# Optimization experiments

Hardware: AMD Instinct MI355X
Metric: run time of the kernel (lower is better)

Reference implementation:

```python
import jax, jax.numpy as jnp
import numpy as np


def _dF(field, c):
    """Central differences of component c of field [B,X,Y,Z,C] -> [B,X-2,Y-2,Z-2,3]."""
    f = field[..., c]
    dx = (f[:, 2:, 1:-1, 1:-1] - f[:, :-2, 1:-1, 1:-1]) * 0.5
    dy = (f[:, 1:-1, 2:, 1:-1] - f[:, 1:-1, :-2, 1:-1]) * 0.5
    dz = (f[:, 1:-1, 1:-1, 2:] - f[:, 1:-1, 1:-1, :-2]) * 0.5
    return jnp.stack((dx, dy, dz), axis=4)


def setup_inputs() -> dict:
    key = jax.random.key(0)
    grid = jax.random.normal(key, (2, 160, 160, 160, 3), dtype=jnp.float32)
    return {"grid": grid}


def reference(grid):
    # First derivatives of each displacement component: [B,X-2,Y-2,Z-2,3]
    dx = _dF(grid, 0)
    dy = _dF(grid, 1)
    dz = _dF(grid, 2)
    # Second derivatives: [B,X-4,Y-4,Z-4,3]
    dxx = _dF(dx, 0)
    dyy = _dF(dy, 1)
    dzz = _dF(dz, 2)
    dxy = _dF(dx, 1)
    dyz = _dF(dy, 2)
    dxz = _dF(dx, 2)
    penalty = jnp.sum(dxx ** 2 + dyy ** 2 + dzz ** 2
                      + 2.0 * (dxy ** 2 + dyz ** 2 + dxz ** 2))
    return penalty / dxx.size
```

## Files before the change

### kernel.cpp

```cpp
#include <hip/hip_runtime.h>

#define OY 480
#define OX 76800
#define SB 12288000
#define JT 12
#define KQ 13
#define IT 12
#define NROW 16
#define ZST 60
#define RST 180
#define SLICE (NROW*RST)
#define CTHR (JT*KQ)
#define NGRP (NROW*14)
#define NBLK 1014
#define INV_SIZE (1.0f/22778496.0f)

__device__ __forceinline__ float4 ld4p(const float* p){ return *reinterpret_cast<const float4*>(p); }
__device__ __forceinline__ float2 ld2p(const float* p){ return *reinterpret_cast<const float2*>(p); }
__device__ __forceinline__ void st4p(float* p, float4 v){ *reinterpret_cast<float4*>(p) = v; }

#define STEP(P, V0a, V0b, DP) { \
    const int s = 2*d + (P); \
    const bool doLoad = stg && (s <= 14); \
    float4 A4, B4, C4; \
    if (doLoad) { \
        const float* gp = G + (size_t)(i0 - 1 + s)*OX + gbase; \
        A4 = ld4p(gp); B4 = ld4p(gp+4); C4 = ld4p(gp+8); \
    } \
    if (act) { \
        const bool doWS = (s >= 2) && (s <= 13); \
        const bool doXY = (s >= 3) && (s <= 14); \
        const bool doXX = (s >= 4); \
        const float* L = lds + (P)*SLICE; \
        float v0c[4], dz0[4], dz1[4], dz2[4], dyc0[4], dyc1[4]; \
        {  \
          float4 lo = ld4p(L+oj), hi = ld4p(L+oj+4); \
          float f[8] = {lo.x,lo.y,lo.z,lo.w,hi.x,hi.y,hi.z,hi.w}; \
          _Pragma("unroll") for (int v=0;v<4;++v){ v0c[v]=f[v+2]; dz0[v]=f[v+3]-f[v+1]; } \
          if (doWS) { \
            _Pragma("unroll") for (int v=0;v<4;++v){ float h=f[v+4]-2.f*f[v+2]+f[v]; cls2=fmaf(h,h,cls2); } \
            float2 pa=ld2p(L+oj+2*RST+2), pb=ld2p(L+oj+2*RST+4); \
            float2 ma=ld2p(L+oj-2*RST+2), mb=ld2p(L+oj-2*RST+4); \
            float hp[4]={pa.x,pa.y,pb.x,pb.y}, hm[4]={ma.x,ma.y,mb.x,mb.y}; \
            _Pragma("unroll") for (int v=0;v<4;++v){ float h=hp[v]-2.f*f[v+2]+hm[v]; cls2=fmaf(h,h,cls2); } \
          } \
        } \
        {  \
          float4 lo = ld4p(L+oj+ZST), hi = ld4p(L+oj+ZST+4); \
          float f[8] = {lo.x,lo.y,lo.z,lo.w,hi.x,hi.y,hi.z,hi.w}; \
          _Pragma("unroll") for (int v=0;v<4;++v){ dz1[v]=f[v+3]-f[v+1]; } \
          if (doWS) { \
            _Pragma("unroll") for (int v=0;v<4;++v){ float h=f[v+4]-2.f*f[v+2]+f[v]; cls2=fmaf(h,h,cls2); } \
            float2 pa=ld2p(L+oj+2*RST+ZST+2), pb=ld2p(L+oj+2*RST+ZST+4); \
            float2 ma=ld2p(L+oj-2*RST+ZST+2), mb=ld2p(L+oj-2*RST+ZST+4); \
            float hp[4]={pa.x,pa.y,pb.x,pb.y}, hm[4]={ma.x,ma.y,mb.x,mb.y}; \
            _Pragma("unroll") for (int v=0;v<4;++v){ float h=hp[v]-2.f*f[v+2]+hm[v]; cls1=fmaf(h,h,cls1); } \
          } \
        } \
        {  \
          float4 lo = ld4p(L+oj+2*ZST), hi = ld4p(L+oj+2*ZST+4); \
          float f[8] = {lo.x,lo.y,lo.z,lo.w,hi.x,hi.y,hi.z,hi.w}; \
          _Pragma("unroll") for (int v=0;v<4;++v){ dz2[v]=f[v+3]-f[v+1]; } \
          if (doWS) { \
            _Pragma("unroll") for (int v=0;v<4;++v){ float h=f[v+4]-2.f*f[v+2]+f[v]; cls1=fmaf(h,h,cls1); } \
          } \
        } \
        {  \
          float4 plo=ld4p(L+oj+RST), phi=ld4p(L+oj+RST+4); \
          float4 mlo=ld4p(L+oj-RST), mhi=ld4p(L+oj-RST+4); \
          float dyw[6]={plo.y-mlo.y, plo.z-mlo.z, plo.w-mlo.w, phi.x-mhi.x, phi.y-mhi.y, phi.z-mhi.z}; \
          _Pragma("unroll") for (int v=0;v<4;++v) dyc0[v]=dyw[v+1]; \
          if (doWS) { _Pragma("unroll") for (int v=0;v<4;++v){ float h=dyw[v+2]-dyw[v]; cls4=fmaf(h,h,cls4); } } \
        } \
        {  \
          float4 plo=ld4p(L+oj+RST+ZST), phi=ld4p(L+oj+RST+ZST+4); \
          float4 mlo=ld4p(L+oj-RST+ZST), mhi=ld4p(L+oj-RST+ZST+4); \
          float dyw[6]={plo.y-mlo.y, plo.z-mlo.z, plo.w-mlo.w, phi.x-mhi.x, phi.y-mhi.y, phi.z-mhi.z}; \
          _Pragma("unroll") for (int v=0;v<4;++v) dyc1[v]=dyw[v+1]; \
          if (doWS) { _Pragma("unroll") for (int v=0;v<4;++v){ float h=dyw[v+2]-dyw[v]; cls3=fmaf(h,h,cls3); } } \
        } \
        if (doWS) {  \
          float4 plo=ld4p(L+oj+RST+2*ZST), phi=ld4p(L+oj+RST+2*ZST+4); \
          float4 mlo=ld4p(L+oj-RST+2*ZST), mhi=ld4p(L+oj-RST+2*ZST+4); \
          float dyw[6]={plo.y-mlo.y, plo.z-mlo.z, plo.w-mlo.w, phi.x-mhi.x, phi.y-mhi.y, phi.z-mhi.z}; \
          _Pragma("unroll") for (int v=0;v<4;++v){ float h=dyw[v+2]-dyw[v]; cls1=fmaf(h,h,cls1); } \
        } \
        _Pragma("unroll") for (int v=0;v<4;++v) { \
          float o0=DP[0][v], o1=DP[1][v], o2=DP[2][v], o3=DP[3][v], o4=DP[4][v]; \
          if (doXY) { float h; \
            h=dyc0[v]-o0; cls3=fmaf(h,h,cls3); \
            h=dyc1[v]-o1; cls1=fmaf(h,h,cls1); \
            h=dz0[v]-o2;  cls3=fmaf(h,h,cls3); \
            h=dz1[v]-o3;  cls2=fmaf(h,h,cls2); \
            h=dz2[v]-o4;  cls1=fmaf(h,h,cls1); \
          } \
          DP[0][v]=dyc0[v]; DP[1][v]=dyc1[v]; DP[2][v]=dz0[v]; DP[3][v]=dz1[v]; DP[4][v]=dz2[v]; \
          float w2v=V0a[v], w4v=V0b[v]; \
          if (doXX) { float h=v0c[v]-2.f*w2v+w4v; cls1=fmaf(h,h,cls1); } \
          V0b[v]=w2v; V0a[v]=v0c[v]; \
        } \
    } \
    if (doLoad) { \
        float* Lw = lds + ((P)^1)*SLICE + lbase; \
        st4p(Lw,       make_float4(A4.x,A4.w,B4.z,C4.y)); \
        st4p(Lw+ZST,   make_float4(A4.y,B4.x,B4.w,C4.z)); \
        st4p(Lw+2*ZST, make_float4(A4.z,B4.y,C4.x,C4.w)); \
    } \
    __syncthreads(); \
}

__global__ __launch_bounds__(256)
void be_partials(const float* __restrict__ g, float* __restrict__ partial) {
    __shared__ float lds[2*SLICE];
    __shared__ float wsum[4];

    const int tid = threadIdx.x;
    const int bid = blockIdx.x;
    const int is = bid % 13;
    int r1 = bid / 13;
    const int kt = r1 % 3; r1 /= 3;
    const int jt = r1 % 13;
    const int bb = r1 / 13;

    const int j0  = 2 + jt*JT;
    const int zlo = 52*kt;
    const int i0  = 2 + is*IT;
    const float* __restrict__ G = g + (size_t)bb*SB;

    const bool stg = tid < NGRP;
    int gbase = 0, lbase = 0;
    if (stg) {
        int rr = tid/14, zq = tid - (tid/14)*14;
        gbase = (j0-2+rr)*OY + (zlo+4*zq)*3;
        lbase = rr*RST + 4*zq;
    }

    const bool act = tid < CTHR;
    int cj = tid/KQ, cq = tid - (tid/KQ)*KQ;
    if (!act) { cj = 0; cq = 0; }
    const int oj = (cj+2)*RST + 4*cq;

    float v0A0[4], v0A1[4], v0B0[4], v0B1[4];
    float dpA[5][4], dpB[5][4];
    #pragma unroll
    for (int v=0;v<4;++v){
        v0A0[v]=v0A1[v]=v0B0[v]=v0B1[v]=0.f;
        #pragma unroll
        for (int q=0;q<5;++q){ dpA[q][v]=0.f; dpB[q][v]=0.f; }
    }
    float cls1=0.f, cls2=0.f, cls3=0.f, cls4=0.f;

    if (stg) {
        const float* gp = G + (size_t)(i0-2)*OX + gbase;
        float4 A4 = ld4p(gp), B4 = ld4p(gp+4), C4 = ld4p(gp+8);
        float* Lw = lds + lbase;
        st4p(Lw,       make_float4(A4.x,A4.w,B4.z,C4.y));
        st4p(Lw+ZST,   make_float4(A4.y,B4.x,B4.w,C4.z));
        st4p(Lw+2*ZST, make_float4(A4.z,B4.y,C4.x,C4.w));
    }
    __syncthreads();

    #pragma unroll 1
    for (int d = 0; d < 8; ++d) {
        STEP(0, v0A0, v0A1, dpA)
        STEP(1, v0B0, v0B1, dpB)
    }

    float sv = fmaf(2.f, cls2, cls1);
    sv = fmaf(3.f, cls3, sv);
    sv = fmaf(4.f, cls4, sv);
    sv *= 0.0625f;

    #pragma unroll
    for (int off = 32; off > 0; off >>= 1) sv += __shfl_down(sv, off, 64);
    if ((tid & 63) == 0) wsum[tid >> 6] = sv;
    __syncthreads();
    if (tid == 0)
        partial[bid] = (wsum[0] + wsum[1]) + (wsum[2] + wsum[3]);
}

__global__ __launch_bounds__(256)
void be_final(const float* __restrict__ partial, float* __restrict__ out) {
    float s = 0.0f;
    for (int i = threadIdx.x; i < NBLK; i += 256) s += partial[i];
    #pragma unroll
    for (int off = 32; off > 0; off >>= 1) s += __shfl_down(s, off, 64);
    __shared__ float ws[4];
    if ((threadIdx.x & 63) == 0) ws[threadIdx.x >> 6] = s;
    __syncthreads();
    if (threadIdx.x == 0)
        out[0] = ((ws[0] + ws[1]) + (ws[2] + ws[3])) * INV_SIZE;
}

extern "C" void kernel_launch(void* const* d_in, const int* in_sizes, int n_in,
                              void* d_out, int out_size, void* d_ws, size_t ws_size,
                              hipStream_t stream) {
    const float* grid = (const float*)d_in[0];
    float* out = (float*)d_out;
    float* partials = (float*)d_ws;

    be_partials<<<dim3(NBLK), dim3(256), 0, stream>>>(grid, partials);
    be_final<<<1, 256, 0, stream>>>(partials, out);
}
```

Before: 177.7 us.

## Keep interleaved xyz layout in LDS and retile to full-Z row blocks

Stops de-interleaving the three displacement components into separate LDS planes and instead copies full contiguous Y-rows (all Z, interleaved components) straight into shared memory with flat float4 copies. Tiles now span the full Z extent with 6 Y-rows per block, giving 676 blocks of 234 compute threads instead of 1014 blocks of 156, with an occupancy hint of 3 blocks per CU. The aim is simpler, fully coalesced staging and better thread utilisation. In exchange each thread does wider LDS reads (24-float vectors), holds more registers, and staging now reads some redundant clamped data.

```diff
diff --git a/kernel.cpp b/kernel.cpp
--- a/kernel.cpp
+++ b/kernel.cpp
@@ -3,160 +3,156 @@
 #define OY 480
 #define OX 76800
 #define SB 12288000
-#define JT 12
-#define KQ 13
+#define JT 6
+#define NROW 10
 #define IT 12
-#define NROW 16
-#define ZST 60
-#define RST 180
-#define SLICE (NROW*RST)
-#define CTHR (JT*KQ)
-#define NGRP (NROW*14)
-#define NBLK 1014
+#define NSEG 13
+#define DATF4 1200
+#define SLICEF 5120
+#define CTHR 234
+#define NBLK 676
 #define INV_SIZE (1.0f/22778496.0f)
 
 __device__ __forceinline__ float4 ld4p(const float* p){ return *reinterpret_cast<const float4*>(p); }
-__device__ __forceinline__ float2 ld2p(const float* p){ return *reinterpret_cast<const float2*>(p); }
 __device__ __forceinline__ void st4p(float* p, float4 v){ *reinterpret_cast<float4*>(p) = v; }
+
+__device__ __forceinline__ void ld24(float* d, const float* p){
+    float4 x0=ld4p(p), x1=ld4p(p+4), x2=ld4p(p+8), x3=ld4p(p+12), x4=ld4p(p+16), x5=ld4p(p+20);
+    d[0]=x0.x; d[1]=x0.y; d[2]=x0.z; d[3]=x0.w;
+    d[4]=x1.x; d[5]=x1.y; d[6]=x1.z; d[7]=x1.w;
+    d[8]=x2.x; d[9]=x2.y; d[10]=x2.z; d[11]=x2.w;
+    d[12]=x3.x; d[13]=x3.y; d[14]=x3.z; d[15]=x3.w;
+    d[16]=x4.x; d[17]=x4.y; d[18]=x4.z; d[19]=x4.w;
+    d[20]=x5.x; d[21]=x5.y; d[22]=x5.z; d[23]=x5.w;
+}
+__device__ __forceinline__ void ld16(float* d, const float* p){
+    float4 x0=ld4p(p), x1=ld4p(p+4), x2=ld4p(p+8), x3=ld4p(p+12);
+    d[0]=x0.x; d[1]=x0.y; d[2]=x0.z; d[3]=x0.w;
+    d[4]=x1.x; d[5]=x1.y; d[6]=x1.z; d[7]=x1.w;
+    d[8]=x2.x; d[9]=x2.y; d[10]=x2.z; d[11]=x2.w;
+    d[12]=x3.x; d[13]=x3.y; d[14]=x3.z; d[15]=x3.w;
+}
 
 #define STEP(P, V0a, V0b, DP) { \
     const int s = 2*d + (P); \
-    const bool doLoad = stg && (s <= 14); \
-    float4 A4, B4, C4; \
+    const bool doLoad = (s <= 14); \
+    float4 a0, a1, a2, a3, a4; \
     if (doLoad) { \
-        const float* gp = G + (size_t)(i0 - 1 + s)*OX + gbase; \
-        A4 = ld4p(gp); B4 = ld4p(gp+4); C4 = ld4p(gp+8); \
+        const float* bp = G + (size_t)(i0 - 1 + s) * OX; \
+        a0 = ld4p(bp+gof0); a1 = ld4p(bp+gof1); a2 = ld4p(bp+gof2); \
+        a3 = ld4p(bp+gof3); a4 = ld4p(bp+gof4); \
     } \
     if (act) { \
         const bool doWS = (s >= 2) && (s <= 13); \
         const bool doXY = (s >= 3) && (s <= 14); \
         const bool doXX = (s >= 4); \
-        const float* L = lds + (P)*SLICE; \
-        float v0c[4], dz0[4], dz1[4], dz2[4], dyc0[4], dyc1[4]; \
-        {  \
-          float4 lo = ld4p(L+oj), hi = ld4p(L+oj+4); \
-          float f[8] = {lo.x,lo.y,lo.z,lo.w,hi.x,hi.y,hi.z,hi.w}; \
-          _Pragma("unroll") for (int v=0;v<4;++v){ v0c[v]=f[v+2]; dz0[v]=f[v+3]-f[v+1]; } \
-          if (doWS) { \
-            _Pragma("unroll") for (int v=0;v<4;++v){ float h=f[v+4]-2.f*f[v+2]+f[v]; cls2=fmaf(h,h,cls2); } \
-            float2 pa=ld2p(L+oj+2*RST+2), pb=ld2p(L+oj+2*RST+4); \
-            float2 ma=ld2p(L+oj-2*RST+2), mb=ld2p(L+oj-2*RST+4); \
-            float hp[4]={pa.x,pa.y,pb.x,pb.y}, hm[4]={ma.x,ma.y,mb.x,mb.y}; \
-            _Pragma("unroll") for (int v=0;v<4;++v){ float h=hp[v]-2.f*f[v+2]+hm[v]; cls2=fmaf(h,h,cls2); } \
-          } \
-        } \
-        {  \
-          float4 lo = ld4p(L+oj+ZST), hi = ld4p(L+oj+ZST+4); \
-          float f[8] = {lo.x,lo.y,lo.z,lo.w,hi.x,hi.y,hi.z,hi.w}; \
-          _Pragma("unroll") for (int v=0;v<4;++v){ dz1[v]=f[v+3]-f[v+1]; } \
-          if (doWS) { \
-            _Pragma("unroll") for (int v=0;v<4;++v){ float h=f[v+4]-2.f*f[v+2]+f[v]; cls2=fmaf(h,h,cls2); } \
-            float2 pa=ld2p(L+oj+2*RST+ZST+2), pb=ld2p(L+oj+2*RST+ZST+4); \
-            float2 ma=ld2p(L+oj-2*RST+ZST+2), mb=ld2p(L+oj-2*RST+ZST+4); \
-            float hp[4]={pa.x,pa.y,pb.x,pb.y}, hm[4]={ma.x,ma.y,mb.x,mb.y}; \
-            _Pragma("unroll") for (int v=0;v<4;++v){ float h=hp[v]-2.f*f[v+2]+hm[v]; cls1=fmaf(h,h,cls1); } \
-          } \
-        } \
-        {  \
-          float4 lo = ld4p(L+oj+2*ZST), hi = ld4p(L+oj+2*ZST+4); \
-          float f[8] = {lo.x,lo.y,lo.z,lo.w,hi.x,hi.y,hi.z,hi.w}; \
-          _Pragma("unroll") for (int v=0;v<4;++v){ dz2[v]=f[v+3]-f[v+1]; } \
-          if (doWS) { \
-            _Pragma("unroll") for (int v=0;v<4;++v){ float h=f[v+4]-2.f*f[v+2]+f[v]; cls1=fmaf(h,h,cls1); } \
-          } \
-        } \
-        {  \
-          float4 plo=ld4p(L+oj+RST), phi=ld4p(L+oj+RST+4); \
-          float4 mlo=ld4p(L+oj-RST), mhi=ld4p(L+oj-RST+4); \
-          float dyw[6]={plo.y-mlo.y, plo.z-mlo.z, plo.w-mlo.w, phi.x-mhi.x, phi.y-mhi.y, phi.z-mhi.z}; \
-          _Pragma("unroll") for (int v=0;v<4;++v) dyc0[v]=dyw[v+1]; \
-          if (doWS) { _Pragma("unroll") for (int v=0;v<4;++v){ float h=dyw[v+2]-dyw[v]; cls4=fmaf(h,h,cls4); } } \
-        } \
-        {  \
-          float4 plo=ld4p(L+oj+RST+ZST), phi=ld4p(L+oj+RST+ZST+4); \
-          float4 mlo=ld4p(L+oj-RST+ZST), mhi=ld4p(L+oj-RST+ZST+4); \
-          float dyw[6]={plo.y-mlo.y, plo.z-mlo.z, plo.w-mlo.w, phi.x-mhi.x, phi.y-mhi.y, phi.z-mhi.z}; \
-          _Pragma("unroll") for (int v=0;v<4;++v) dyc1[v]=dyw[v+1]; \
-          if (doWS) { _Pragma("unroll") for (int v=0;v<4;++v){ float h=dyw[v+2]-dyw[v]; cls3=fmaf(h,h,cls3); } } \
-        } \
-        if (doWS) {  \
-          float4 plo=ld4p(L+oj+RST+2*ZST), phi=ld4p(L+oj+RST+2*ZST+4); \
-          float4 mlo=ld4p(L+oj-RST+2*ZST), mhi=ld4p(L+oj-RST+2*ZST+4); \
-          float dyw[6]={plo.y-mlo.y, plo.z-mlo.z, plo.w-mlo.w, phi.x-mhi.x, phi.y-mhi.y, phi.z-mhi.z}; \
-          _Pragma("unroll") for (int v=0;v<4;++v){ float h=dyw[v+2]-dyw[v]; cls1=fmaf(h,h,cls1); } \
-        } \
-        _Pragma("unroll") for (int v=0;v<4;++v) { \
-          float o0=DP[0][v], o1=DP[1][v], o2=DP[2][v], o3=DP[3][v], o4=DP[4][v]; \
-          if (doXY) { float h; \
-            h=dyc0[v]-o0; cls3=fmaf(h,h,cls3); \
-            h=dyc1[v]-o1; cls1=fmaf(h,h,cls1); \
-            h=dz0[v]-o2;  cls3=fmaf(h,h,cls3); \
-            h=dz1[v]-o3;  cls2=fmaf(h,h,cls2); \
-            h=dz2[v]-o4;  cls1=fmaf(h,h,cls1); \
-          } \
-          DP[0][v]=dyc0[v]; DP[1][v]=dyc1[v]; DP[2][v]=dz0[v]; DP[3][v]=dz1[v]; DP[4][v]=dz2[v]; \
-          float w2v=V0a[v], w4v=V0b[v]; \
-          if (doXX) { float h=v0c[v]-2.f*w2v+w4v; cls1=fmaf(h,h,cls1); } \
-          V0b[v]=w2v; V0a[v]=v0c[v]; \
+        const float* Lr = lds + (P)*SLICEF + oj; \
+        float fcn[24]; ld24(fcn, Lr); \
+        float v0c[4], dzc0[4], dzc1[4], dzc2[4]; \
+        _Pragma("unroll") for (int v=0; v<4; ++v) { \
+            v0c[v]  = fcn[6+3*v]; \
+            dzc0[v] = fcn[9+3*v]  - fcn[3+3*v]; \
+            dzc1[v] = fcn[10+3*v] - fcn[4+3*v]; \
+            dzc2[v] = fcn[11+3*v] - fcn[5+3*v]; \
+        } \
+        if (doWS) { \
+            _Pragma("unroll") for (int v=0; v<4; ++v) { \
+                float h0 = fcn[12+3*v] - 2.f*fcn[6+3*v] + fcn[3*v];   cls2 = fmaf(h0,h0,cls2); \
+                float h1 = fcn[13+3*v] - 2.f*fcn[7+3*v] + fcn[1+3*v]; cls2 = fmaf(h1,h1,cls2); \
+                float h2 = fcn[14+3*v] - 2.f*fcn[8+3*v] + fcn[2+3*v]; cls1 = fmaf(h2,h2,cls1); \
+            } \
+            float p2[16], m2[16]; \
+            ld16(p2, Lr + 2*OY + 4); \
+            ld16(m2, Lr - 2*OY + 4); \
+            _Pragma("unroll") for (int v=0; v<4; ++v) { \
+                float h0 = p2[2+3*v] - 2.f*fcn[6+3*v] + m2[2+3*v]; cls2 = fmaf(h0,h0,cls2); \
+                float h1 = p2[3+3*v] - 2.f*fcn[7+3*v] + m2[3+3*v]; cls1 = fmaf(h1,h1,cls1); \
+            } \
+        } \
+        float fp[24], fm[24]; \
+        ld24(fp, Lr + OY); ld24(fm, Lr - OY); \
+        float dyc0[4], dyc1[4]; \
+        _Pragma("unroll") for (int v=0; v<4; ++v) { \
+            dyc0[v] = fp[3*(v+2)]   - fm[3*(v+2)]; \
+            dyc1[v] = fp[3*(v+2)+1] - fm[3*(v+2)+1]; \
+        } \
+        if (doWS) { \
+            _Pragma("unroll") for (int v=0; v<4; ++v) { \
+                float ha = (fp[3*(v+3)]   - fm[3*(v+3)])   - (fp[3*(v+1)]   - fm[3*(v+1)]);   cls4 = fmaf(ha,ha,cls4); \
+                float hb = (fp[3*(v+3)+1] - fm[3*(v+3)+1]) - (fp[3*(v+1)+1] - fm[3*(v+1)+1]); cls3 = fmaf(hb,hb,cls3); \
+                float hc = (fp[3*(v+3)+2] - fm[3*(v+3)+2]) - (fp[3*(v+1)+2] - fm[3*(v+1)+2]); cls1 = fmaf(hc,hc,cls1); \
+            } \
+        } \
+        _Pragma("unroll") for (int v=0; v<4; ++v) { \
+            if (doXY) { float h; \
+                h = dyc0[v] - DP[0][v]; cls3 = fmaf(h,h,cls3); \
+                h = dyc1[v] - DP[1][v]; cls1 = fmaf(h,h,cls1); \
+                h = dzc0[v] - DP[2][v]; cls3 = fmaf(h,h,cls3); \
+                h = dzc1[v] - DP[3][v]; cls2 = fmaf(h,h,cls2); \
+                h = dzc2[v] - DP[4][v]; cls1 = fmaf(h,h,cls1); \
+            } \
+            DP[0][v] = dyc0[v]; DP[1][v] = dyc1[v]; \
+            DP[2][v] = dzc0[v]; DP[3][v] = dzc1[v]; DP[4][v] = dzc2[v]; \
+            float w2v = V0a[v], w4v = V0b[v]; \
+            if (doXX) { float h = v0c[v] - 2.f*w2v + w4v; cls1 = fmaf(h,h,cls1); } \
+            V0b[v] = w2v; V0a[v] = v0c[v]; \
         } \
     } \
     if (doLoad) { \
-        float* Lw = lds + ((P)^1)*SLICE + lbase; \
-        st4p(Lw,       make_float4(A4.x,A4.w,B4.z,C4.y)); \
-        st4p(Lw+ZST,   make_float4(A4.y,B4.x,B4.w,C4.z)); \
-        st4p(Lw+2*ZST, make_float4(A4.z,B4.y,C4.x,C4.w)); \
+        float* Lw = lds + ((P)^1)*SLICEF; \
+        st4p(Lw+lof0, a0); st4p(Lw+lof1, a1); st4p(Lw+lof2, a2); \
+        st4p(Lw+lof3, a3); st4p(Lw+lof4, a4); \
     } \
     __syncthreads(); \
 }
 
-__global__ __launch_bounds__(256)
+__global__ __launch_bounds__(256, 3)
 void be_partials(const float* __restrict__ g, float* __restrict__ partial) {
-    __shared__ float lds[2*SLICE];
+    __shared__ float lds[2*SLICEF];
     __shared__ float wsum[4];
 
     const int tid = threadIdx.x;
     const int bid = blockIdx.x;
-    const int is = bid % 13;
-    int r1 = bid / 13;
-    const int kt = r1 % 3; r1 /= 3;
-    const int jt = r1 % 13;
-    const int bb = r1 / 13;
-
-    const int j0  = 2 + jt*JT;
-    const int zlo = 52*kt;
-    const int i0  = 2 + is*IT;
-    const float* __restrict__ G = g + (size_t)bb*SB;
-
-    const bool stg = tid < NGRP;
-    int gbase = 0, lbase = 0;
-    if (stg) {
-        int rr = tid/14, zq = tid - (tid/14)*14;
-        gbase = (j0-2+rr)*OY + (zlo+4*zq)*3;
-        lbase = rr*RST + 4*zq;
+    const int is = bid % NSEG;
+    int r1 = bid / NSEG;
+    const int jt = r1 % 26;
+    const int bb = r1 / 26;
+
+    const int j0 = 2 + jt*JT;
+    const int i0 = 2 + is*IT;
+    const float* __restrict__ G = g + (size_t)bb*SB + (size_t)(j0-2)*OY;
+
+    int gof0, gof1, gof2, gof3, gof4, lof0, lof1, lof2, lof3, lof4;
+    {
+        int f;
+        f = tid;          gof0 = 4*(f < DATF4 ? f : DATF4-1); lof0 = 4*f;
+        f = tid + 256;    gof1 = 4*(f < DATF4 ? f : DATF4-1); lof1 = 4*f;
+        f = tid + 512;    gof2 = 4*(f < DATF4 ? f : DATF4-1); lof2 = 4*f;
+        f = tid + 768;    gof3 = 4*(f < DATF4 ? f : DATF4-1); lof3 = 4*f;
+        f = tid + 1024;   gof4 = 4*(f < DATF4 ? f : DATF4-1); lof4 = 4*f;
     }
 
     const bool act = tid < CTHR;
-    int cj = tid/KQ, cq = tid - (tid/KQ)*KQ;
+    int cj = tid / 39, cq = tid - (tid/39)*39;
     if (!act) { cj = 0; cq = 0; }
-    const int oj = (cj+2)*RST + 4*cq;
+    const int oj = (cj+2)*OY + 12*cq;
 
     float v0A0[4], v0A1[4], v0B0[4], v0B1[4];
     float dpA[5][4], dpB[5][4];
     #pragma unroll
-    for (int v=0;v<4;++v){
+    for (int v=0; v<4; ++v) {
         v0A0[v]=v0A1[v]=v0B0[v]=v0B1[v]=0.f;
         #pragma unroll
-        for (int q=0;q<5;++q){ dpA[q][v]=0.f; dpB[q][v]=0.f; }
+        for (int q=0; q<5; ++q) { dpA[q][v]=0.f; dpB[q][v]=0.f; }
     }
     float cls1=0.f, cls2=0.f, cls3=0.f, cls4=0.f;
 
-    if (stg) {
-        const float* gp = G + (size_t)(i0-2)*OX + gbase;
-        float4 A4 = ld4p(gp), B4 = ld4p(gp+4), C4 = ld4p(gp+8);
-        float* Lw = lds + lbase;
-        st4p(Lw,       make_float4(A4.x,A4.w,B4.z,C4.y));
-        st4p(Lw+ZST,   make_float4(A4.y,B4.x,B4.w,C4.z));
-        st4p(Lw+2*ZST, make_float4(A4.z,B4.y,C4.x,C4.w));
+    {
+        const float* bp = G + (size_t)(i0-2)*OX;
+        float4 a0=ld4p(bp+gof0), a1=ld4p(bp+gof1), a2=ld4p(bp+gof2),
+               a3=ld4p(bp+gof3), a4=ld4p(bp+gof4);
+        st4p(lds+lof0, a0); st4p(lds+lof1, a1); st4p(lds+lof2, a2);
+        st4p(lds+lof3, a3); st4p(lds+lof4, a4);
     }
     __syncthreads();
 
```

After: 164.5 us. 7.4% less time.
